# Kernel optimization log

Measured on AMD Instinct MI355X. Metric: run time of the kernel, lower is better.

The kernel has to match this reference:

```python
import jax, jax.numpy as jnp
import numpy as np

B, T, D_F, L = 64, 256, 32, 128

def setup_inputs() -> dict:
    key = jax.random.key(0)
    k1, k2, k3, k4, k5 = jax.random.split(key, 5)
    return {
        "x": jax.random.normal(k1, (B, T, D_F), dtype=jnp.float32),
        "latent": jax.random.normal(k2, (B, T, L), dtype=jnp.float32),
        "kernel": jax.random.normal(k3, (1, 1, D_F, L), dtype=jnp.float32) * (6.0 / (D_F + L)) ** 0.5,
        "bias": jax.random.uniform(k4, (1, 1, D_F, L), dtype=jnp.float32),
        "unnorm_beta": jax.random.uniform(k5, (1, T, 1), dtype=jnp.float32),
    }

def reference(x, latent, kernel, bias, unnorm_beta):
    # features: [B,T,D_f,L]
    features = jax.nn.relu(x[..., None] * kernel + bias)
    # normal equations: X^T X over latent axis -> [B,T,D_f,D_f]
    xtx = jnp.einsum('btdl,btel->btde', features, features)
    xtx_inv = jnp.linalg.inv(xtx)
    # X^T y: [B,T,D_f]
    xty = jnp.einsum('btdl,btl->btd', features, latent)
    scores = jnp.einsum('btde,bte->btd', xtx_inv, xty)  # [B,T,D_f]
    # o_hat: weighted sum of feature rows -> [B,T,L]
    o_hat = jnp.einsum('btd,btdl->btl', scores, features)
    # L1-normalized attention over time: [1,T,1]
    abs_b = jnp.abs(unnorm_beta)
    weights = abs_b / jnp.sum(abs_b, axis=1)
    return jnp.sum(o_hat * weights, axis=1)  # [B,L]
```

## Files before the change

### kernel.cpp

```cpp
#include <hip/hip_runtime.h>
#include <stdint.h>

#define B_ 64
#define T_ 256
#define DF 32
#define L_ 128
#define AW 34
#define SLICE 4352

typedef float  v2f    __attribute__((ext_vector_type(2)));
typedef float  f32x16 __attribute__((ext_vector_type(16)));
typedef short  bf16x8 __attribute__((ext_vector_type(8)));

#define WAVE_SYNC() do { asm volatile("s_waitcnt lgkmcnt(0)" ::: "memory"); \
                         __builtin_amdgcn_sched_barrier(0); } while (0)

template <int IMM>
__device__ __forceinline__ float swz_f(float v) {
    return __builtin_bit_cast(float, __builtin_amdgcn_ds_swizzle(
        __builtin_bit_cast(int, v), IMM));
}
__device__ __forceinline__ uint32_t cvt_pk_bf16(float a, float b) {
    uint32_t r;
    asm("v_cvt_pk_bf16_f32 %0, %1, %2" : "=v"(r) : "v"(a), "v"(b));
    return r;
}
__device__ __forceinline__ float lo_f(uint32_t p) { return __builtin_bit_cast(float, p << 16); }
__device__ __forceinline__ float hi_f(uint32_t p) { return __builtin_bit_cast(float, p & 0xFFFF0000u); }

struct frag3 { bf16x8 h, m, l; };
union U8 { uint32_t u[4]; bf16x8 v; };

__device__ __forceinline__ frag3 split3(float4 a, float4 b) {
    uint32_t h0 = cvt_pk_bf16(a.x, a.y), h1 = cvt_pk_bf16(a.z, a.w);
    uint32_t h2 = cvt_pk_bf16(b.x, b.y), h3 = cvt_pk_bf16(b.z, b.w);
    float e0 = a.x - lo_f(h0), e1 = a.y - hi_f(h0);
    float e2 = a.z - lo_f(h1), e3 = a.w - hi_f(h1);
    float e4 = b.x - lo_f(h2), e5 = b.y - hi_f(h2);
    float e6 = b.z - lo_f(h3), e7 = b.w - hi_f(h3);
    uint32_t m0 = cvt_pk_bf16(e0, e1), m1 = cvt_pk_bf16(e2, e3);
    uint32_t m2 = cvt_pk_bf16(e4, e5), m3 = cvt_pk_bf16(e6, e7);
    float g0 = e0 - lo_f(m0), g1 = e1 - hi_f(m0);
    float g2 = e2 - lo_f(m1), g3 = e3 - hi_f(m1);
    float g4 = e4 - lo_f(m2), g5 = e5 - hi_f(m2);
    float g6 = e6 - lo_f(m3), g7 = e7 - hi_f(m3);
    uint32_t l0 = cvt_pk_bf16(g0, g1), l1 = cvt_pk_bf16(g2, g3);
    uint32_t l2 = cvt_pk_bf16(g4, g5), l3 = cvt_pk_bf16(g6, g7);
    U8 H, M, L;
    H.u[0] = h0; H.u[1] = h1; H.u[2] = h2; H.u[3] = h3;
    M.u[0] = m0; M.u[1] = m1; M.u[2] = m2; M.u[3] = m3;
    L.u[0] = l0; L.u[1] = l1; L.u[2] = l2; L.u[3] = l3;
    frag3 r; r.h = H.v; r.m = M.v; r.l = L.v; return r;
}

__device__ __forceinline__ f32x16 mfma32(bf16x8 a, bf16x8 b, f32x16 c) {
    return __builtin_amdgcn_mfma_f32_32x32x16_bf16(a, b, c, 0, 0, 0);
}

template <int K>
__device__ __forceinline__ void gj_round(float (&A)[33], float& dinv, int r) {
    float piv = swz_f<(K << 5)>(A[K]);
    float ip = __builtin_amdgcn_rcpf(piv);
    ip = ip * (2.0f - piv * ip);
    const bool isk = (r == K);
    float fmul = isk ? 0.f : A[K] * ip;
    dinv = isk ? ip : dinv;
    #pragma unroll
    for (int m = K + 1; m < 33; ++m) {
        float pk = swz_f<(K << 5)>(A[m]);
        A[m] = fmaf(-fmul, pk, A[m]);
    }
}

template <int K>
struct GJ {
    static __device__ __forceinline__ void run(float (&A)[33], float& dinv, int r) {
        gj_round<K>(A, dinv, r);
        GJ<K + 1>::run(A, dinv, r);
    }
};
template <>
struct GJ<32> {
    static __device__ __forceinline__ void run(float (&)[33], float&, int) {}
};

__global__ __launch_bounds__(64) void feat_kernel(
    const float* __restrict__ x,
    const float* __restrict__ latent,
    const float* __restrict__ kern,
    const float* __restrict__ bias,
    const float* __restrict__ beta,
    float* __restrict__ out,
    int mode)
{
    __shared__ __align__(16) char smem[2 * SLICE];
    const int lane = threadIdx.x;
    const int btA  = blockIdx.x * 2;
    const int btB  = btA + 1;

    const int g = lane >> 5;
    const int r = lane & 31;

    float* AsA = reinterpret_cast<float*>(smem);
    float* AsB = reinterpret_cast<float*>(smem + SLICE);

    const float4* kern4 = reinterpret_cast<const float4*>(kern);
    const float4* bias4 = reinterpret_cast<const float4*>(bias);
    const float4* latA4 = reinterpret_cast<const float4*>(latent) + (size_t)btA * 32;
    const float4* latB4 = reinterpret_cast<const float4*>(latent) + (size_t)btB * 32;

    const float xA = x[(size_t)btA * DF + r];
    const float xB = x[(size_t)btB * DF + r];

    f32x16 GA, GB;
    #pragma unroll
    for (int i = 0; i < 16; ++i) { GA[i] = 0.f; GB[i] = 0.f; }
    float ayA = 0.f, ayB = 0.f;

    #pragma unroll 2
    for (int ks = 0; ks < 8; ++ks) {
        const int idx = r * 32 + ks * 4 + g * 2;
        float4 Ka = kern4[idx],  Kb = kern4[idx + 1];
        float4 Ba = bias4[idx],  Bb = bias4[idx + 1];

        float4 faA, fbA, faB, fbB;
        faA.x = fmaxf(fmaf(xA, Ka.x, Ba.x), 0.f);
        faA.y = fmaxf(fmaf(xA, Ka.y, Ba.y), 0.f);
        faA.z = fmaxf(fmaf(xA, Ka.z, Ba.z), 0.f);
        faA.w = fmaxf(fmaf(xA, Ka.w, Ba.w), 0.f);
        fbA.x = fmaxf(fmaf(xA, Kb.x, Bb.x), 0.f);
        fbA.y = fmaxf(fmaf(xA, Kb.y, Bb.y), 0.f);
        fbA.z = fmaxf(fmaf(xA, Kb.z, Bb.z), 0.f);
        fbA.w = fmaxf(fmaf(xA, Kb.w, Bb.w), 0.f);
        faB.x = fmaxf(fmaf(xB, Ka.x, Ba.x), 0.f);
        faB.y = fmaxf(fmaf(xB, Ka.y, Ba.y), 0.f);
        faB.z = fmaxf(fmaf(xB, Ka.z, Ba.z), 0.f);
        faB.w = fmaxf(fmaf(xB, Ka.w, Ba.w), 0.f);
        fbB.x = fmaxf(fmaf(xB, Kb.x, Bb.x), 0.f);
        fbB.y = fmaxf(fmaf(xB, Kb.y, Bb.y), 0.f);
        fbB.z = fmaxf(fmaf(xB, Kb.z, Bb.z), 0.f);
        fbB.w = fmaxf(fmaf(xB, Kb.w, Bb.w), 0.f);

        float4 laA = latA4[ks * 4 + g * 2], lbA = latA4[ks * 4 + g * 2 + 1];
        float4 laB = latB4[ks * 4 + g * 2], lbB = latB4[ks * 4 + g * 2 + 1];
        ayA = fmaf(faA.x, laA.x, ayA); ayA = fmaf(faA.y, laA.y, ayA);
        ayA = fmaf(faA.z, laA.z, ayA); ayA = fmaf(faA.w, laA.w, ayA);
        ayA = fmaf(fbA.x, lbA.x, ayA); ayA = fmaf(fbA.y, lbA.y, ayA);
        ayA = fmaf(fbA.z, lbA.z, ayA); ayA = fmaf(fbA.w, lbA.w, ayA);
        ayB = fmaf(faB.x, laB.x, ayB); ayB = fmaf(faB.y, laB.y, ayB);
        ayB = fmaf(faB.z, laB.z, ayB); ayB = fmaf(faB.w, laB.w, ayB);
        ayB = fmaf(fbB.x, lbB.x, ayB); ayB = fmaf(fbB.y, lbB.y, ayB);
        ayB = fmaf(fbB.z, lbB.z, ayB); ayB = fmaf(fbB.w, lbB.w, ayB);

        frag3 FA = split3(faA, fbA);
        frag3 FB = split3(faB, fbB);
        GA = mfma32(FA.h, FA.h, GA);
        GB = mfma32(FB.h, FB.h, GB);
        GA = mfma32(FA.h, FA.m, GA);
        GB = mfma32(FB.h, FB.m, GB);
        GA = mfma32(FA.m, FA.h, GA);
        GB = mfma32(FB.m, FB.h, GB);
        GA = mfma32(FA.h, FA.l, GA);
        GB = mfma32(FB.h, FB.l, GB);
        GA = mfma32(FA.l, FA.h, GA);
        GB = mfma32(FB.l, FB.h, GB);
        GA = mfma32(FA.m, FA.m, GA);
        GB = mfma32(FB.m, FB.m, GB);
    }
    ayA += __shfl_xor(ayA, 32);
    ayB += __shfl_xor(ayB, 32);

    #pragma unroll
    for (int reg = 0; reg < 16; ++reg) {
        const int row = (reg & 3) + 8 * (reg >> 2) + 4 * g;
        AsA[row * AW + r] = GA[reg];
        AsB[row * AW + r] = GB[reg];
    }
    if (g == 0) AsA[r * AW + 32] = ayA;
    else        AsB[r * AW + 32] = ayB;
    WAVE_SYNC();

    float A[33];
    {
        const float* Amy = g ? AsB : AsA;
        #pragma unroll
        for (int m = 0; m < 16; ++m) {
            v2f t = *reinterpret_cast<const v2f*>(&Amy[r * AW + 2 * m]);
            A[2 * m]     = t[0];
            A[2 * m + 1] = t[1];
        }
        A[32] = Amy[r * AW + 32];
    }

    float dinv = 0.f;
    GJ<0>::run(A, dinv, r);
    const float s = A[32] * dinv;

    {
        float4 oA = make_float4(0.f, 0.f, 0.f, 0.f);
        float4 oB = make_float4(0.f, 0.f, 0.f, 0.f);
        #pragma unroll
        for (int dd = 0; dd < 16; ++dd) {
            int d = g * 16 + dd;
            float4 K  = kern4[d * 32 + r];
            float4 Bv = bias4[d * 32 + r];
            float xvA = __shfl(xA, d);
            float xvB = __shfl(xB, d);
            float sA  = __shfl(s, d);
            float sB  = __shfl(s, 32 + d);
            float fx = fmaxf(fmaf(xvA, K.x, Bv.x), 0.f);
            float fy = fmaxf(fmaf(xvA, K.y, Bv.y), 0.f);
            float fz = fmaxf(fmaf(xvA, K.z, Bv.z), 0.f);
            float fw = fmaxf(fmaf(xvA, K.w, Bv.w), 0.f);
            oA.x = fmaf(sA, fx, oA.x);
            oA.y = fmaf(sA, fy, oA.y);
            oA.z = fmaf(sA, fz, oA.z);
            oA.w = fmaf(sA, fw, oA.w);
            fx = fmaxf(fmaf(xvB, K.x, Bv.x), 0.f);
            fy = fmaxf(fmaf(xvB, K.y, Bv.y), 0.f);
            fz = fmaxf(fmaf(xvB, K.z, Bv.z), 0.f);
            fw = fmaxf(fmaf(xvB, K.w, Bv.w), 0.f);
            oB.x = fmaf(sB, fx, oB.x);
            oB.y = fmaf(sB, fy, oB.y);
            oB.z = fmaf(sB, fz, oB.z);
            oB.w = fmaf(sB, fw, oB.w);
        }
        oA.x += __shfl_xor(oA.x, 32); oA.y += __shfl_xor(oA.y, 32);
        oA.z += __shfl_xor(oA.z, 32); oA.w += __shfl_xor(oA.w, 32);
        oB.x += __shfl_xor(oB.x, 32); oB.y += __shfl_xor(oB.y, 32);
        oB.z += __shfl_xor(oB.z, 32); oB.w += __shfl_xor(oB.w, 32);

        if (mode == 0) {
            if (g == 0) reinterpret_cast<float4*>(out)[(size_t)btA * 32 + r] = oA;
            else        reinterpret_cast<float4*>(out)[(size_t)btB * 32 + r] = oB;
        } else {
            float v = fabsf(beta[lane]) + fabsf(beta[lane + 64]) +
                      fabsf(beta[lane + 128]) + fabsf(beta[lane + 192]);
            #pragma unroll
            for (int off = 32; off > 0; off >>= 1) v += __shfl_down(v, off);
            float S = __shfl(v, 0);
            const int tA = btA & (T_ - 1), tB = btB & (T_ - 1);
            const int b  = btA >> 8;
            if (g == 0) {
                float w_t = fabsf(beta[tA]) / S;
                float* op = &out[(size_t)b * L_ + 4 * r];
                atomicAdd(op + 0, oA.x * w_t);
                atomicAdd(op + 1, oA.y * w_t);
                atomicAdd(op + 2, oA.z * w_t);
                atomicAdd(op + 3, oA.w * w_t);
            } else {
                float w_t = fabsf(beta[tB]) / S;
                float* op = &out[(size_t)b * L_ + 4 * r];
                atomicAdd(op + 0, oB.x * w_t);
                atomicAdd(op + 1, oB.y * w_t);
                atomicAdd(op + 2, oB.z * w_t);
                atomicAdd(op + 3, oB.w * w_t);
            }
        }
    }
}

__global__ __launch_bounds__(256) void reduce_kernel(
    const float* __restrict__ ws,
    const float* __restrict__ beta,
    float* __restrict__ out)
{
    __shared__ float wsh[T_];
    __shared__ __align__(16) float4 par[8][32];
    __shared__ float red[4];
    const int b = blockIdx.x, tid = threadIdx.x;

    float bv = fabsf(beta[tid]);
    wsh[tid] = bv;
    float v = bv;
    #pragma unroll
    for (int o = 32; o > 0; o >>= 1) v += __shfl_down(v, o);
    if ((tid & 63) == 0) red[tid >> 6] = v;
    __syncthreads();
    const float S = red[0] + red[1] + red[2] + red[3];

    const int c = tid & 31, gg = tid >> 5;
    const float4* ws4 = reinterpret_cast<const float4*>(ws);
    float4 a = make_float4(0.f, 0.f, 0.f, 0.f);
    #pragma unroll 4
    for (int tt = 0; tt < 32; ++tt) {
        int t = gg * 32 + tt;
        float w = wsh[t];
        float4 u = ws4[((size_t)b * T_ + t) * 32 + c];
        a.x = fmaf(u.x, w, a.x);
        a.y = fmaf(u.y, w, a.y);
        a.z = fmaf(u.z, w, a.z);
        a.w = fmaf(u.w, w, a.w);
    }
    par[gg][c] = a;
    __syncthreads();
    if (tid < 32) {
        float4 s = par[0][tid];
        #pragma unroll
        for (int p = 1; p < 8; ++p) {
            float4 u = par[p][tid];
            s.x += u.x; s.y += u.y; s.z += u.z; s.w += u.w;
        }
        float inv = 1.0f / S;
        s.x *= inv; s.y *= inv; s.z *= inv; s.w *= inv;
        reinterpret_cast<float4*>(out)[b * 32 + tid] = s;
    }
}

extern "C" void kernel_launch(void* const* d_in, const int* in_sizes, int n_in,
                              void* d_out, int out_size, void* d_ws, size_t ws_size,
                              hipStream_t stream) {
    const float* x      = (const float*)d_in[0];
    const float* latent = (const float*)d_in[1];
    const float* kern   = (const float*)d_in[2];
    const float* bias   = (const float*)d_in[3];
    const float* beta   = (const float*)d_in[4];
    float* out = (float*)d_out;

    const size_t need = (size_t)B_ * T_ * L_ * sizeof(float);
    if (ws_size >= need) {
        float* ws = (float*)d_ws;
        feat_kernel<<<(B_ * T_) / 2, 64, 0, stream>>>(x, latent, kern, bias, beta, ws, 0);
        reduce_kernel<<<B_, 256, 0, stream>>>(ws, beta, out);
    } else {
        (void)hipMemsetAsync(d_out, 0, (size_t)out_size * sizeof(float), stream);
        feat_kernel<<<(B_ * T_) / 2, 64, 0, stream>>>(x, latent, kern, bias, beta, out, 1);
    }
}
```

Baseline: 72.20 us.

## Use packed FP32 FMAs, drop Newton refinement of pivot reciprocal, set min waves

Rewrites the feature-generation, X^T y accumulation and output accumulation loops to use v_pk_fma_f32 on pairs of floats, roughly halving the VALU FMA instruction count. It also removes the Newton-Raphson refinement step after the hardware reciprocal in the Gauss-Jordan pivot. It adds a minimum-blocks hint to launch_bounds to limit register use. Dropping the refinement reduces pivot precision, which may affect accuracy of the inverse, and the packed ops may add register moves for operand packing.

```diff
diff --git a/kernel.cpp b/kernel.cpp
--- a/kernel.cpp
+++ b/kernel.cpp
@@ -20,6 +20,11 @@
     return __builtin_bit_cast(float, __builtin_amdgcn_ds_swizzle(
         __builtin_bit_cast(int, v), IMM));
 }
+__device__ __forceinline__ v2f pk_fma(v2f a, v2f b, v2f c) {
+    v2f d;
+    asm("v_pk_fma_f32 %0, %1, %2, %3" : "=v"(d) : "v"(a), "v"(b), "v"(c));
+    return d;
+}
 __device__ __forceinline__ uint32_t cvt_pk_bf16(float a, float b) {
     uint32_t r;
     asm("v_cvt_pk_bf16_f32 %0, %1, %2" : "=v"(r) : "v"(a), "v"(b));
@@ -31,13 +36,13 @@
 struct frag3 { bf16x8 h, m, l; };
 union U8 { uint32_t u[4]; bf16x8 v; };
 
-__device__ __forceinline__ frag3 split3(float4 a, float4 b) {
-    uint32_t h0 = cvt_pk_bf16(a.x, a.y), h1 = cvt_pk_bf16(a.z, a.w);
-    uint32_t h2 = cvt_pk_bf16(b.x, b.y), h3 = cvt_pk_bf16(b.z, b.w);
-    float e0 = a.x - lo_f(h0), e1 = a.y - hi_f(h0);
-    float e2 = a.z - lo_f(h1), e3 = a.w - hi_f(h1);
-    float e4 = b.x - lo_f(h2), e5 = b.y - hi_f(h2);
-    float e6 = b.z - lo_f(h3), e7 = b.w - hi_f(h3);
+__device__ __forceinline__ frag3 split3(v2f p0, v2f p1, v2f p2, v2f p3) {
+    uint32_t h0 = cvt_pk_bf16(p0[0], p0[1]), h1 = cvt_pk_bf16(p1[0], p1[1]);
+    uint32_t h2 = cvt_pk_bf16(p2[0], p2[1]), h3 = cvt_pk_bf16(p3[0], p3[1]);
+    float e0 = p0[0] - lo_f(h0), e1 = p0[1] - hi_f(h0);
+    float e2 = p1[0] - lo_f(h1), e3 = p1[1] - hi_f(h1);
+    float e4 = p2[0] - lo_f(h2), e5 = p2[1] - hi_f(h2);
+    float e6 = p3[0] - lo_f(h3), e7 = p3[1] - hi_f(h3);
     uint32_t m0 = cvt_pk_bf16(e0, e1), m1 = cvt_pk_bf16(e2, e3);
     uint32_t m2 = cvt_pk_bf16(e4, e5), m3 = cvt_pk_bf16(e6, e7);
     float g0 = e0 - lo_f(m0), g1 = e1 - hi_f(m0);
@@ -61,7 +66,6 @@
 __device__ __forceinline__ void gj_round(float (&A)[33], float& dinv, int r) {
     float piv = swz_f<(K << 5)>(A[K]);
     float ip = __builtin_amdgcn_rcpf(piv);
-    ip = ip * (2.0f - piv * ip);
     const bool isk = (r == K);
     float fmul = isk ? 0.f : A[K] * ip;
     dinv = isk ? ip : dinv;
@@ -84,7 +88,7 @@
     static __device__ __forceinline__ void run(float (&)[33], float&, int) {}
 };
 
-__global__ __launch_bounds__(64) void feat_kernel(
+__global__ __launch_bounds__(64, 4) void feat_kernel(
     const float* __restrict__ x,
     const float* __restrict__ latent,
     const float* __restrict__ kern,
@@ -111,49 +115,49 @@
 
     const float xA = x[(size_t)btA * DF + r];
     const float xB = x[(size_t)btB * DF + r];
+    const v2f xA2 = {xA, xA}, xB2 = {xB, xB};
 
     f32x16 GA, GB;
     #pragma unroll
     for (int i = 0; i < 16; ++i) { GA[i] = 0.f; GB[i] = 0.f; }
-    float ayA = 0.f, ayB = 0.f;
+    v2f ayA2 = {0.f, 0.f}, ayB2 = {0.f, 0.f};
 
     #pragma unroll 2
     for (int ks = 0; ks < 8; ++ks) {
         const int idx = r * 32 + ks * 4 + g * 2;
         float4 Ka = kern4[idx],  Kb = kern4[idx + 1];
         float4 Ba = bias4[idx],  Bb = bias4[idx + 1];
-
-        float4 faA, fbA, faB, fbB;
-        faA.x = fmaxf(fmaf(xA, Ka.x, Ba.x), 0.f);
-        faA.y = fmaxf(fmaf(xA, Ka.y, Ba.y), 0.f);
-        faA.z = fmaxf(fmaf(xA, Ka.z, Ba.z), 0.f);
-        faA.w = fmaxf(fmaf(xA, Ka.w, Ba.w), 0.f);
-        fbA.x = fmaxf(fmaf(xA, Kb.x, Bb.x), 0.f);
-        fbA.y = fmaxf(fmaf(xA, Kb.y, Bb.y), 0.f);
-        fbA.z = fmaxf(fmaf(xA, Kb.z, Bb.z), 0.f);
-        fbA.w = fmaxf(fmaf(xA, Kb.w, Bb.w), 0.f);
-        faB.x = fmaxf(fmaf(xB, Ka.x, Ba.x), 0.f);
-        faB.y = fmaxf(fmaf(xB, Ka.y, Ba.y), 0.f);
-        faB.z = fmaxf(fmaf(xB, Ka.z, Ba.z), 0.f);
-        faB.w = fmaxf(fmaf(xB, Ka.w, Ba.w), 0.f);
-        fbB.x = fmaxf(fmaf(xB, Kb.x, Bb.x), 0.f);
-        fbB.y = fmaxf(fmaf(xB, Kb.y, Bb.y), 0.f);
-        fbB.z = fmaxf(fmaf(xB, Kb.z, Bb.z), 0.f);
-        fbB.w = fmaxf(fmaf(xB, Kb.w, Bb.w), 0.f);
+        v2f K0 = {Ka.x, Ka.y}, K1 = {Ka.z, Ka.w};
+        v2f K2 = {Kb.x, Kb.y}, K3 = {Kb.z, Kb.w};
+        v2f B0 = {Ba.x, Ba.y}, B1 = {Ba.z, Ba.w};
+        v2f B2 = {Bb.x, Bb.y}, B3 = {Bb.z, Bb.w};
+
+        v2f a0 = pk_fma(xA2, K0, B0), a1 = pk_fma(xA2, K1, B1);
+        v2f a2 = pk_fma(xA2, K2, B2), a3 = pk_fma(xA2, K3, B3);
+        a0[0] = fmaxf(a0[0], 0.f); a0[1] = fmaxf(a0[1], 0.f);
+        a1[0] = fmaxf(a1[0], 0.f); a1[1] = fmaxf(a1[1], 0.f);
+        a2[0] = fmaxf(a2[0], 0.f); a2[1] = fmaxf(a2[1], 0.f);
+        a3[0] = fmaxf(a3[0], 0.f); a3[1] = fmaxf(a3[1], 0.f);
+        v2f b0 = pk_fma(xB2, K0, B0), b1 = pk_fma(xB2, K1, B1);
+        v2f b2 = pk_fma(xB2, K2, B2), b3 = pk_fma(xB2, K3, B3);
+        b0[0] = fmaxf(b0[0], 0.f); b0[1] = fmaxf(b0[1], 0.f);
+        b1[0] = fmaxf(b1[0], 0.f); b1[1] = fmaxf(b1[1], 0.f);
+        b2[0] = fmaxf(b2[0], 0.f); b2[1] = fmaxf(b2[1], 0.f);
+        b3[0] = fmaxf(b3[0], 0.f); b3[1] = fmaxf(b3[1], 0.f);
 
         float4 laA = latA4[ks * 4 + g * 2], lbA = latA4[ks * 4 + g * 2 + 1];
         float4 laB = latB4[ks * 4 + g * 2], lbB = latB4[ks * 4 + g * 2 + 1];
-        ayA = fmaf(faA.x, laA.x, ayA); ayA = fmaf(faA.y, laA.y, ayA);
-        ayA = fmaf(faA.z, laA.z, ayA); ayA = fmaf(faA.w, laA.w, ayA);
-        ayA = fmaf(fbA.x, lbA.x, ayA); ayA = fmaf(fbA.y, lbA.y, ayA);
-        ayA = fmaf(fbA.z, lbA.z, ayA); ayA = fmaf(fbA.w, lbA.w, ayA);
-        ayB = fmaf(faB.x, laB.x, ayB); ayB = fmaf(faB.y, laB.y, ayB);
-        ayB = fmaf(faB.z, laB.z, ayB); ayB = fmaf(faB.w, laB.w, ayB);
-        ayB = fmaf(fbB.x, lbB.x, ayB); ayB = fmaf(fbB.y, lbB.y, ayB);
-        ayB = fmaf(fbB.z, lbB.z, ayB); ayB = fmaf(fbB.w, lbB.w, ayB);
-
-        frag3 FA = split3(faA, fbA);
-        frag3 FB = split3(faB, fbB);
+        v2f lA0 = {laA.x, laA.y}, lA1 = {laA.z, laA.w};
+        v2f lA2 = {lbA.x, lbA.y}, lA3 = {lbA.z, lbA.w};
+        v2f lB0 = {laB.x, laB.y}, lB1 = {laB.z, laB.w};
+        v2f lB2 = {lbB.x, lbB.y}, lB3 = {lbB.z, lbB.w};
+        ayA2 = pk_fma(a0, lA0, ayA2); ayA2 = pk_fma(a1, lA1, ayA2);
+        ayA2 = pk_fma(a2, lA2, ayA2); ayA2 = pk_fma(a3, lA3, ayA2);
+        ayB2 = pk_fma(b0, lB0, ayB2); ayB2 = pk_fma(b1, lB1, ayB2);
+        ayB2 = pk_fma(b2, lB2, ayB2); ayB2 = pk_fma(b3, lB3, ayB2);
+
+        frag3 FA = split3(a0, a1, a2, a3);
+        frag3 FB = split3(b0, b1, b2, b3);
         GA = mfma32(FA.h, FA.h, GA);
         GB = mfma32(FB.h, FB.h, GB);
         GA = mfma32(FA.h, FA.m, GA);
@@ -167,6 +171,8 @@
         GA = mfma32(FA.m, FA.m, GA);
         GB = mfma32(FB.m, FB.m, GB);
     }
+    float ayA = ayA2[0] + ayA2[1];
+    float ayB = ayB2[0] + ayB2[1];
     ayA += __shfl_xor(ayA, 32);
     ayB += __shfl_xor(ayB, 32);
 
@@ -197,34 +203,36 @@
     const float s = A[32] * dinv;
 
     {
-        float4 oA = make_float4(0.f, 0.f, 0.f, 0.f);
-        float4 oB = make_float4(0.f, 0.f, 0.f, 0.f);
+        v2f oA01 = {0.f, 0.f}, oA23 = {0.f, 0.f};
+        v2f oB01 = {0.f, 0.f}, oB23 = {0.f, 0.f};
         #pragma unroll
         for (int dd = 0; dd < 16; ++dd) {
             int d = g * 16 + dd;
             float4 K  = kern4[d * 32 + r];
             float4 Bv = bias4[d * 32 + r];
+            v2f K01 = {K.x, K.y},  K23 = {K.z, K.w};
+            v2f Bv01 = {Bv.x, Bv.y}, Bv23 = {Bv.z, Bv.w};
             float xvA = __shfl(xA, d);
             float xvB = __shfl(xB, d);
-            float sA  = __shfl(s, d);
-            float sB  = __shfl(s, 32 + d);
-            float fx = fmaxf(fmaf(xvA, K.x, Bv.x), 0.f);
-            float fy = fmaxf(fmaf(xvA, K.y, Bv.y), 0.f);
-            float fz = fmaxf(fmaf(xvA, K.z, Bv.z), 0.f);
-            float fw = fmaxf(fmaf(xvA, K.w, Bv.w), 0.f);
-            oA.x = fmaf(sA, fx, oA.x);
-            oA.y = fmaf(sA, fy, oA.y);
-            oA.z = fmaf(sA, fz, oA.z);
-            oA.w = fmaf(sA, fw, oA.w);
-            fx = fmaxf(fmaf(xvB, K.x, Bv.x), 0.f);
-            fy = fmaxf(fmaf(xvB, K.y, Bv.y), 0.f);
-            fz = fmaxf(fmaf(xvB, K.z, Bv.z), 0.f);
-            fw = fmaxf(fmaf(xvB, K.w, Bv.w), 0.f);
-            oB.x = fmaf(sB, fx, oB.x);
-            oB.y = fmaf(sB, fy, oB.y);
-            oB.z = fmaf(sB, fz, oB.z);
-            oB.w = fmaf(sB, fw, oB.w);
+            v2f xvA2 = {xvA, xvA}, xvB2 = {xvB, xvB};
+            float sA = __shfl(s, d);
+            float sB = __shfl(s, 32 + d);
+            v2f sA2 = {sA, sA}, sB2 = {sB, sB};
+            v2f f01 = pk_fma(xvA2, K01, Bv01);
+            v2f f23 = pk_fma(xvA2, K23, Bv23);
+            f01[0] = fmaxf(f01[0], 0.f); f01[1] = fmaxf(f01[1], 0.f);
+            f23[0] = fmaxf(f23[0], 0.f); f23[1] = fmaxf(f23[1], 0.f);
+            oA01 = pk_fma(sA2, f01, oA01);
+            oA23 = pk_fma(sA2, f23, oA23);
+            f01 = pk_fma(xvB2, K01, Bv01);
+            f23 = pk_fma(xvB2, K23, Bv23);
+            f01[0] = fmaxf(f01[0], 0.f); f01[1] = fmaxf(f01[1], 0.f);
+            f23[0] = fmaxf(f23[0], 0.f); f23[1] = fmaxf(f23[1], 0.f);
+            oB01 = pk_fma(sB2, f01, oB01);
+            oB23 = pk_fma(sB2, f23, oB23);
         }
+        float4 oA = make_float4(oA01[0], oA01[1], oA23[0], oA23[1]);
+        float4 oB = make_float4(oB01[0], oB01[1], oB23[0], oB23[1]);
         oA.x += __shfl_xor(oA.x, 32); oA.y += __shfl_xor(oA.y, 32);
         oA.z += __shfl_xor(oA.z, 32); oA.w += __shfl_xor(oA.w, 32);
         oB.x += __shfl_xor(oB.x, 32); oB.y += __shfl_xor(oB.y, 32);
@@ -241,16 +249,15 @@
             float S = __shfl(v, 0);
             const int tA = btA & (T_ - 1), tB = btB & (T_ - 1);
             const int b  = btA >> 8;
+            float* op = &out[(size_t)b * L_ + 4 * r];
             if (g == 0) {
                 float w_t = fabsf(beta[tA]) / S;
-                float* op = &out[(size_t)b * L_ + 4 * r];
                 atomicAdd(op + 0, oA.x * w_t);
                 atomicAdd(op + 1, oA.y * w_t);
                 atomicAdd(op + 2, oA.z * w_t);
                 atomicAdd(op + 3, oA.w * w_t);
             } else {
                 float w_t = fabsf(beta[tB]) / S;
-                float* op = &out[(size_t)b * L_ + 4 * r];
                 atomicAdd(op + 0, oB.x * w_t);
                 atomicAdd(op + 1, oB.y * w_t);
                 atomicAdd(op + 2, oB.z * w_t);
```

Result: faster. 68.34 us (-5.3%).
